# Optimization experiments

Measured on AMD Instinct MI355X. Metric: run time of the kernel, lower is better.

Reference implementation:

```python
import jax, jax.numpy as jnp
import numpy as np

N_EMBD = 1024
N_HEAD = 16
HEAD_DIM = N_EMBD // N_HEAD


def setup_inputs() -> dict:
    key = jax.random.key(0)
    kx, kq, kk, kv, ko = jax.random.split(key, 5)
    B, S = 2, 2048
    return {
        "x": jax.random.normal(kx, (B, S, N_EMBD), dtype=jnp.float32),
        "W_q": jax.random.normal(kq, (N_EMBD, N_EMBD), dtype=jnp.float32),
        "W_k": jax.random.normal(kk, (N_EMBD, N_EMBD), dtype=jnp.float32),
        "W_v": jax.random.normal(kv, (N_EMBD, N_EMBD), dtype=jnp.float32),
        "W_o": jax.random.normal(ko, (N_EMBD, N_EMBD), dtype=jnp.float32),
    }


def reference(x, W_q, W_k, W_v, W_o):
    B, S, E = x.shape
    H, D = N_HEAD, HEAD_DIM
    scale = 1.0 / np.sqrt(D).astype(np.float32)
    # QKV projections, split into heads: (B, H, S, D)
    q = (x @ W_q).reshape(B, S, H, D).transpose(0, 2, 1, 3)
    k = (x @ W_k).reshape(B, S, H, D).transpose(0, 2, 1, 3)
    v = (x @ W_v).reshape(B, S, H, D).transpose(0, 2, 1, 3)
    # scaled scores with causal mask
    scores = jnp.einsum("bhqd,bhkd->bhqk", q, k) * scale
    causal = jnp.tril(jnp.ones((S, S), dtype=bool))
    scores = jnp.where(causal, scores, -jnp.inf)
    attn = jax.nn.softmax(scores, axis=-1)
    out = jnp.einsum("bhqk,bhkd->bhqd", attn, v)
    out = out.transpose(0, 2, 1, 3).reshape(B, S, E)
    return out @ W_o
```

## Files before the change

kernel.cpp:

```cpp
#include <hip/hip_runtime.h>
#include <stdint.h>

#define E 1024
#define S 2048
#define NH 16
#define HD 64

typedef _Float16 f16;
typedef _Float16 f16x4 __attribute__((ext_vector_type(4)));
typedef _Float16 f16x8 __attribute__((ext_vector_type(8)));
typedef __fp16 hv4 __attribute__((ext_vector_type(4)));
typedef float f32x4 __attribute__((ext_vector_type(4)));

__device__ __forceinline__ void async16(const void* g, void* l) {
  __builtin_amdgcn_global_load_lds(
      (const __attribute__((address_space(1))) unsigned int*)g,
      (__attribute__((address_space(3))) unsigned int*)l, 16, 0, 0);
}

__global__ __launch_bounds__(256) void cvt_all(
    const float* __restrict__ x, const float* __restrict__ Wq,
    const float* __restrict__ Wk, const float* __restrict__ Wv,
    const float* __restrict__ Wo, f16* __restrict__ xh, f16* __restrict__ xl,
    f16* __restrict__ Wh, f16* __restrict__ Wl) {
  const int z = blockIdx.z;
  const int tid = threadIdx.x;
  if (z == 4) {
    int base = ((blockIdx.y * 32 + blockIdx.x) * 256 + tid) * 16;
#pragma unroll
    for (int u = 0; u < 4; u++) {
      int i = base + u * 4;
      float4 a = *(const float4*)(x + i);
      f16 h0 = (f16)a.x, h1 = (f16)a.y, h2 = (f16)a.z, h3 = (f16)a.w;
      f16x4 hv = {h0, h1, h2, h3};
      f16x4 lv = {(f16)(a.x - (float)h0), (f16)(a.y - (float)h1),
                  (f16)(a.z - (float)h2), (f16)(a.w - (float)h3)};
      *(f16x4*)(xh + i) = hv;
      *(f16x4*)(xl + i) = lv;
    }
    return;
  }
  __shared__ float tile[32][33];
  const float* W = z == 0 ? Wq : z == 1 ? Wk : z == 2 ? Wv : Wo;
  const int tx = tid & 31, ty = tid >> 5;
  const int x0 = blockIdx.x * 32, y0 = blockIdx.y * 32;
#pragma unroll
  for (int i = 0; i < 4; i++)
    tile[ty + i * 8][tx] = W[(size_t)(y0 + ty + i * 8) * E + x0 + tx];
  __syncthreads();
  f16* outh = Wh + (size_t)z * E * E;
  f16* outl = Wl + (size_t)z * E * E;
#pragma unroll
  for (int i = 0; i < 4; i++) {
    float v = tile[tx][ty + i * 8];
    size_t o = (size_t)(x0 + ty + i * 8) * E + (y0 + tx);
    f16 hi = (f16)v;
    outh[o] = hi;
    if (z < 2) outl[o] = (f16)(v - (float)hi);
  }
}


template <bool SPLIT2>
__device__ __forceinline__ void gemm_mainloop(
    const f16* __restrict__ Ah, const f16* __restrict__ Al,
    const f16* __restrict__ Bh, const f16* __restrict__ Bl, int m0, int n0,
    int K, f16* Ahs, f16* Als, f16* Bhs, f16* Bls, f32x4 acc[4][4]) {
  const int tid = threadIdx.x, lane = tid & 63, wid = tid >> 6;
  const int quad = lane >> 4, c16 = lane & 15;
  const int rA = tid >> 2;
  const int cA = (tid & 3) ^ ((rA >> 1) & 3);
  const size_t gA0 = (size_t)(m0 + rA) * K + cA * 8;
  const size_t gA1 = (size_t)(m0 + 64 + rA) * K + cA * 8;
  const size_t gB0 = (size_t)(n0 + rA) * K + cA * 8;
  const size_t gB1 = (size_t)(n0 + 64 + rA) * K + cA * 8;
  const int l0 = tid * 8, l1 = (256 + tid) * 8;
  int a_off[4], b_off[4];
#pragma unroll
  for (int i = 0; i < 4; i++) {
    int ra = (wid >> 1) * 64 + i * 16 + c16;
    a_off[i] = ra * 32 + ((quad ^ ((ra >> 1) & 3)) << 3);
    int rb = (wid & 1) * 64 + i * 16 + c16;
    b_off[i] = rb * 32 + ((quad ^ ((rb >> 1) & 3)) << 3);
  }
  auto stage = [&](int k0, int b) {
    const int o = b << 12;
    async16(Ah + gA0 + k0, Ahs + o + l0);
    async16(Ah + gA1 + k0, Ahs + o + l1);
    async16(Bh + gB0 + k0, Bhs + o + l0);
    async16(Bh + gB1 + k0, Bhs + o + l1);
    if constexpr (SPLIT2) {
      async16(Al + gA0 + k0, Als + o + l0);
      async16(Al + gA1 + k0, Als + o + l1);
      async16(Bl + gB0 + k0, Bls + o + l0);
      async16(Bl + gB1 + k0, Bls + o + l1);
    }
  };
  stage(0, 0);
  int cur = 0;
  for (int k0 = 0; k0 < K; k0 += 32, cur ^= 1) {
    __syncthreads();
    if (k0 + 32 < K) stage(k0 + 32, cur ^ 1);
    const int o = cur << 12;
    f16x8 ah[4], bh[4];
#pragma unroll
    for (int i = 0; i < 4; i++) {
      ah[i] = *(const f16x8*)(Ahs + o + a_off[i]);
      bh[i] = *(const f16x8*)(Bhs + o + b_off[i]);
    }
    if constexpr (SPLIT2) {
      f16x8 al[4], bl[4];
#pragma unroll
      for (int i = 0; i < 4; i++) {
        al[i] = *(const f16x8*)(Als + o + a_off[i]);
        bl[i] = *(const f16x8*)(Bls + o + b_off[i]);
      }
#pragma unroll
      for (int i = 0; i < 4; i++)
#pragma unroll
        for (int j = 0; j < 4; j++) {
          acc[i][j] = __builtin_amdgcn_mfma_f32_16x16x32_f16(ah[i], bh[j], acc[i][j], 0, 0, 0);
          acc[i][j] = __builtin_amdgcn_mfma_f32_16x16x32_f16(ah[i], bl[j], acc[i][j], 0, 0, 0);
          acc[i][j] = __builtin_amdgcn_mfma_f32_16x16x32_f16(al[i], bh[j], acc[i][j], 0, 0, 0);
        }
    } else {
#pragma unroll
      for (int i = 0; i < 4; i++)
#pragma unroll
        for (int j = 0; j < 4; j++)
          acc[i][j] = __builtin_amdgcn_mfma_f32_16x16x32_f16(ah[i], bh[j], acc[i][j], 0, 0, 0);
    }
  }
}

__global__ __launch_bounds__(256) void qkv_gemm(
    const f16* __restrict__ xh, const f16* __restrict__ xl,
    const f16* __restrict__ Wh, const f16* __restrict__ Wl,
    f16* __restrict__ Qh, f16* __restrict__ Ql, f16* __restrict__ Kh,
    f16* __restrict__ Kl, f16* __restrict__ Vt) {
  __shared__ __align__(16) f16 Ahs[2][4096], Als[2][4096], Bhs[2][4096],
      Bls[2][4096];
  const int z = blockIdx.y >> 3;
  const int m0 = blockIdx.x * 128, n0 = (blockIdx.y & 7) * 128;
  const f16* Bth = Wh + (size_t)z * E * E;
  const f16* Btl = Wl + (size_t)z * E * E;
  f32x4 acc[4][4];
  const f32x4 zero4 = {0.f, 0.f, 0.f, 0.f};
#pragma unroll
  for (int i = 0; i < 4; i++)
#pragma unroll
    for (int j = 0; j < 4; j++) acc[i][j] = zero4;
  if (z < 2)
    gemm_mainloop<true>(xh, xl, Bth, Btl, m0, n0, E, &Ahs[0][0], &Als[0][0],
                        &Bhs[0][0], &Bls[0][0], acc);
  else
    gemm_mainloop<false>(xh, nullptr, Bth, nullptr, m0, n0, E, &Ahs[0][0],
                         nullptr, &Bhs[0][0], nullptr, acc);
  const int tid = threadIdx.x, lane = tid & 63, wid = tid >> 6;
  const int quad = lane >> 4, c16 = lane & 15;
  if (z == 2) {
    __syncthreads();
    f16* vbuf = &Ahs[0][0] + (size_t)wid * 4608;
#pragma unroll
    for (int i = 0; i < 4; i++)
#pragma unroll
      for (int j = 0; j < 4; j++)
#pragma unroll
        for (int r = 0; r < 4; r++) {
          int sl = i * 16 + quad * 4 + r;
          int dl = j * 16 + c16;
          vbuf[dl * 72 + sl] = (f16)acc[i][j][r];
        }
#pragma unroll
    for (int i2 = 0; i2 < 8; i2++) {
      int dl = i2 * 8 + (lane >> 3);
      int ck = lane & 7;
      f16x8 v8 = *(const f16x8*)(vbuf + dl * 72 + ck * 8);
      int dg = n0 + (wid & 1) * 64 + dl;
      int sg = m0 + (wid >> 1) * 64 + ck * 8;
      int b = sg >> 11, s = sg & (S - 1);
      int h = dg >> 6, d = dg & 63;
      *(f16x8*)(Vt + (((size_t)(b * NH + h) * HD + d) << 11) + s) = v8;
    }
  } else {
    const float sc = 0.42466090014400953f;
#pragma unroll
    for (int i = 0; i < 4; i++)
#pragma unroll
      for (int j = 0; j < 4; j++)
#pragma unroll
        for (int r = 0; r < 4; r++) {
          int row = m0 + (wid >> 1) * 64 + i * 16 + quad * 4 + r;
          int col = n0 + (wid & 1) * 64 + j * 16 + c16;
          int b = row >> 11, s = row & (S - 1);
          int h = col >> 6, d = col & 63;
          float v = acc[i][j][r] * sc;
          size_t idx = (((size_t)(b * NH + h) * S + s) << 6) + d;
          f16 hi = (f16)v;
          f16 lo = (f16)(v - (float)hi);
          if (z == 0) { Qh[idx] = hi; Ql[idx] = lo; }
          else        { Kh[idx] = hi; Kl[idx] = lo; }
        }
  }
}

__global__ __launch_bounds__(256, 3) void flash(
    const f16* __restrict__ Qh, const f16* __restrict__ Ql,
    const f16* __restrict__ Kh, const f16* __restrict__ Kl,
    const f16* __restrict__ Vt, f16* __restrict__ Ao) {
  __shared__ __align__(16) f16 Khs[2][4096], Kls[2][4096], Vs[2][4096];
  const int tid = threadIdx.x, lane = tid & 63, wid = tid >> 6;
  const int quad = lane >> 4, c16 = lane & 15;
  const int flat = blockIdx.y * 32 + blockIdx.x;
  const int xcd = flat & 7, slot = flat >> 3;
  const int bh = xcd * 4 + (slot >> 5);
  const int qtile = 31 - (slot & 31);
  const int q0 = qtile * 64;
  const size_t bhoff = (size_t)bh * S * HD;
  const int qbase = wid * 16;
  f16x8 qf_h[2], qf_l[2];
#pragma unroll
  for (int ks = 0; ks < 2; ks++) {
    int q = q0 + qbase + c16;
    size_t off = bhoff + (size_t)q * HD + ks * 32 + quad * 8;
    qf_h[ks] = *(const f16x8*)(Qh + off);
    qf_l[ks] = *(const f16x8*)(Ql + off);
  }
  const int niter = qtile + 1;
  const int s0 = tid, s1 = 256 + tid;
  const int r0 = s0 >> 3, cc0 = ((s0 & 7) ^ (r0 & 7)) * 8;
  const int r1 = s1 >> 3, cc1 = ((s1 & 7) ^ (r1 & 7)) * 8;
  auto stage = [&](int it, int b) {
    const size_t kb = bhoff + (size_t)(it * 64) * HD;
    async16(Kh + kb + r0 * HD + cc0, &Khs[b][s0 * 8]);
    async16(Kh + kb + r1 * HD + cc1, &Khs[b][s1 * 8]);
    async16(Kl + kb + r0 * HD + cc0, &Kls[b][s0 * 8]);
    async16(Kl + kb + r1 * HD + cc1, &Kls[b][s1 * 8]);
    const size_t vb = bhoff + (size_t)(it * 64);
    async16(Vt + vb + (size_t)r0 * S + cc0, &Vs[b][s0 * 8]);
    async16(Vt + vb + (size_t)r1 * S + cc1, &Vs[b][s1 * 8]);
  };
  stage(0, 0);
  float mrow = -3.0e38f, lsum = 0.f;
  f32x4 oacc[4];
  const f32x4 zero4 = {0.f, 0.f, 0.f, 0.f};
#pragma unroll
  for (int dt = 0; dt < 4; dt++) oacc[dt] = zero4;
  const int qrow = q0 + qbase + c16;
  for (int it = 0; it < niter; ++it) {
    const int cur = it & 1;
    __syncthreads();
    if (it + 1 < niter) stage(it + 1, cur ^ 1);
    const int k0 = it * 64;
    f32x4 st[4];
#pragma unroll
    for (int kt = 0; kt < 4; kt++) st[kt] = zero4;
#pragma unroll
    for (int kt = 0; kt < 4; kt++) {
      int rowk = (kt * 16 + c16) * 64;
      int sx = c16 & 7;
      f16x8 kh0 = *(const f16x8*)&Khs[cur][rowk + ((quad ^ sx) << 3)];
      f16x8 kh1 = *(const f16x8*)&Khs[cur][rowk + (((4 + quad) ^ sx) << 3)];
      f16x8 kl0 = *(const f16x8*)&Kls[cur][rowk + ((quad ^ sx) << 3)];
      f16x8 kl1 = *(const f16x8*)&Kls[cur][rowk + (((4 + quad) ^ sx) << 3)];
      st[kt] = __builtin_amdgcn_mfma_f32_16x16x32_f16(kh0, qf_h[0], st[kt], 0, 0, 0);
      st[kt] = __builtin_amdgcn_mfma_f32_16x16x32_f16(kh1, qf_h[1], st[kt], 0, 0, 0);
      st[kt] = __builtin_amdgcn_mfma_f32_16x16x32_f16(kh0, qf_l[0], st[kt], 0, 0, 0);
      st[kt] = __builtin_amdgcn_mfma_f32_16x16x32_f16(kh1, qf_l[1], st[kt], 0, 0, 0);
      st[kt] = __builtin_amdgcn_mfma_f32_16x16x32_f16(kl0, qf_h[0], st[kt], 0, 0, 0);
      st[kt] = __builtin_amdgcn_mfma_f32_16x16x32_f16(kl1, qf_h[1], st[kt], 0, 0, 0);
    }
    if (it == niter - 1) {
#pragma unroll
      for (int kt = 0; kt < 4; kt++) {
        int kb = k0 + kt * 16 + quad * 4;
#pragma unroll
        for (int r = 0; r < 4; r++)
          if (kb + r > qrow) st[kt][r] = -3.0e38f;
      }
    }
    float mx = -3.0e38f;
#pragma unroll
    for (int kt = 0; kt < 4; kt++) {
      float a = fmaxf(fmaxf(st[kt][0], st[kt][1]), fmaxf(st[kt][2], st[kt][3]));
      mx = fmaxf(mx, a);
    }
    mx = fmaxf(mx, __shfl_xor(mx, 16, 64));
    mx = fmaxf(mx, __shfl_xor(mx, 32, 64));
    float mn = fmaxf(mrow, mx);
    float alpha = __builtin_amdgcn_exp2f(mrow - mn);
    mrow = mn;
    float ls = lsum * alpha;
    hv4 pb[4];
#pragma unroll
    for (int kt = 0; kt < 4; kt++) {
      float p0 = __builtin_amdgcn_exp2f(st[kt][0] - mn);
      float p1 = __builtin_amdgcn_exp2f(st[kt][1] - mn);
      float p2 = __builtin_amdgcn_exp2f(st[kt][2] - mn);
      float p3 = __builtin_amdgcn_exp2f(st[kt][3] - mn);
      ls += (p0 + p1) + (p2 + p3);
      hv4 pv = {(__fp16)p0, (__fp16)p1, (__fp16)p2, (__fp16)p3};
      pb[kt] = pv;
    }
    lsum = ls;
#pragma unroll
    for (int dt = 0; dt < 4; dt++) {
      oacc[dt][0] *= alpha;
      oacc[dt][1] *= alpha;
      oacc[dt][2] *= alpha;
      oacc[dt][3] *= alpha;
    }
#pragma unroll
    for (int kt = 0; kt < 4; kt++) {
#pragma unroll
      for (int dt = 0; dt < 4; dt++) {
        int rowd = dt * 16 + c16;
        int cidx = (kt * 2 + (quad >> 1)) ^ (rowd & 7);
        hv4 vf = *(const hv4*)&Vs[cur][rowd * 64 + (cidx << 3) + (quad & 1) * 4];
        oacc[dt] = __builtin_amdgcn_mfma_f32_16x16x16f16(vf, pb[kt], oacc[dt], 0, 0, 0);
      }
    }
  }
  const int bb = bh >> 4, hh = bh & 15;
  float l = lsum;
  l += __shfl_xor(l, 16, 64);
  l += __shfl_xor(l, 32, 64);
  float iv = 1.0f / l;
  const int q = q0 + qbase + c16;
#pragma unroll
  for (int dt = 0; dt < 4; dt++) {
    f16x4 ov = {(f16)(oacc[dt][0] * iv), (f16)(oacc[dt][1] * iv),
                (f16)(oacc[dt][2] * iv), (f16)(oacc[dt][3] * iv)};
    *(f16x4*)(Ao + ((size_t)(bb * S + q)) * E + hh * 64 + dt * 16 + quad * 4) = ov;
  }
}

__global__ __launch_bounds__(256) void out_gemm(const f16* __restrict__ Ao,
                                                const f16* __restrict__ Wo,
                                                float* __restrict__ Cout) {
  __shared__ __align__(16) f16 Ahs[2][2048], Bhs[2][4096];
  const int tid = threadIdx.x, lane = tid & 63, wid = tid >> 6;
  const int quad = lane >> 4, c16 = lane & 15;
  const int m0 = blockIdx.x * 64, n0 = blockIdx.y * 128;
  f32x4 acc[4][2];
  const f32x4 zero4 = {0.f, 0.f, 0.f, 0.f};
#pragma unroll
  for (int i = 0; i < 4; i++)
#pragma unroll
    for (int j = 0; j < 2; j++) acc[i][j] = zero4;
  const int rA = tid >> 2;
  const int cA = (tid & 3) ^ ((rA >> 1) & 3);
  const size_t gA0 = (size_t)(m0 + rA) * E + cA * 8;
  const size_t gB0 = (size_t)(n0 + rA) * E + cA * 8;
  const size_t gB1 = (size_t)(n0 + 64 + rA) * E + cA * 8;
  const int l0 = tid * 8, l1 = (256 + tid) * 8;
  int a_off[4], b_off[2];
#pragma unroll
  for (int i = 0; i < 4; i++) {
    int ra = i * 16 + c16;
    a_off[i] = ra * 32 + ((quad ^ ((ra >> 1) & 3)) << 3);
  }
#pragma unroll
  for (int j = 0; j < 2; j++) {
    int rb = wid * 32 + j * 16 + c16;
    b_off[j] = rb * 32 + ((quad ^ ((rb >> 1) & 3)) << 3);
  }
  auto stage = [&](int k0, int b) {
    async16(Ao + gA0 + k0, &Ahs[b][0] + l0);
    async16(Wo + gB0 + k0, &Bhs[b][0] + l0);
    async16(Wo + gB1 + k0, &Bhs[b][0] + l1);
  };
  stage(0, 0);
  int cur = 0;
  for (int k0 = 0; k0 < E; k0 += 32, cur ^= 1) {
    __syncthreads();
    if (k0 + 32 < E) stage(k0 + 32, cur ^ 1);
    f16x8 ah[4], bh[2];
#pragma unroll
    for (int i = 0; i < 4; i++) ah[i] = *(const f16x8*)(&Ahs[cur][0] + a_off[i]);
#pragma unroll
    for (int j = 0; j < 2; j++) bh[j] = *(const f16x8*)(&Bhs[cur][0] + b_off[j]);
#pragma unroll
    for (int i = 0; i < 4; i++)
#pragma unroll
      for (int j = 0; j < 2; j++)
        acc[i][j] = __builtin_amdgcn_mfma_f32_16x16x32_f16(ah[i], bh[j], acc[i][j], 0, 0, 0);
  }
#pragma unroll
  for (int i = 0; i < 4; i++)
#pragma unroll
    for (int j = 0; j < 2; j++)
#pragma unroll
      for (int r = 0; r < 4; r++) {
        int row = m0 + i * 16 + quad * 4 + r;
        int col = n0 + wid * 32 + j * 16 + c16;
        Cout[(size_t)row * E + col] = acc[i][j][r];
      }
}

extern "C" void kernel_launch(void* const* d_in, const int* in_sizes, int n_in,
                              void* d_out, int out_size, void* d_ws,
                              size_t ws_size, hipStream_t stream) {
  const float* x = (const float*)d_in[0];
  const float* Wq = (const float*)d_in[1];
  const float* Wk = (const float*)d_in[2];
  const float* Wv = (const float*)d_in[3];
  const float* Wo = (const float*)d_in[4];
  char* ws = (char*)d_ws;
  const size_t MB = (size_t)1 << 20;
  f16* xh = (f16*)(ws + 0 * MB);
  f16* xl = (f16*)(ws + 8 * MB);
  f16* Wh = (f16*)(ws + 16 * MB);
  f16* Wl = (f16*)(ws + 24 * MB);
  f16* Qh = (f16*)(ws + 28 * MB);
  f16* Ql = (f16*)(ws + 36 * MB);
  f16* Kh = (f16*)(ws + 44 * MB);
  f16* Kl = (f16*)(ws + 52 * MB);
  f16* Vt = (f16*)(ws + 60 * MB);
  f16* Ao = (f16*)(ws + 68 * MB);
  cvt_all<<<dim3(32, 32, 5), 256, 0, stream>>>(x, Wq, Wk, Wv, Wo, xh, xl, Wh, Wl);
  qkv_gemm<<<dim3(32, 24), 256, 0, stream>>>(xh, xl, Wh, Wl, Qh, Ql, Kh, Kl, Vt);
  flash<<<dim3(32, 32), 256, 0, stream>>>(Qh, Ql, Kh, Kl, Vt, Ao);
  out_gemm<<<dim3(64, 8), 256, 0, stream>>>(Ao, Wh + (size_t)3 * E * E, (float*)d_out);
}
```

Baseline: 236.4 us.

## Pair complementary causal query tiles per flash block to balance work and share K/V

```diff
diff --git a/kernel.cpp b/kernel.cpp
--- a/kernel.cpp
+++ b/kernel.cpp
@@ -204,29 +204,31 @@
   }
 }
 
-__global__ __launch_bounds__(256, 3) void flash(
+__global__ __launch_bounds__(256, 2) void flash(
     const f16* __restrict__ Qh, const f16* __restrict__ Ql,
     const f16* __restrict__ Kh, const f16* __restrict__ Kl,
     const f16* __restrict__ Vt, f16* __restrict__ Ao) {
   __shared__ __align__(16) f16 Khs[2][4096], Kls[2][4096], Vs[2][4096];
   const int tid = threadIdx.x, lane = tid & 63, wid = tid >> 6;
   const int quad = lane >> 4, c16 = lane & 15;
-  const int flat = blockIdx.y * 32 + blockIdx.x;
+  const int flat = blockIdx.y * 16 + blockIdx.x;
   const int xcd = flat & 7, slot = flat >> 3;
-  const int bh = xcd * 4 + (slot >> 5);
-  const int qtile = 31 - (slot & 31);
-  const int q0 = qtile * 64;
+  const int bh = xcd * 4 + (slot >> 4);
+  const int t = slot & 15;
+  const int q0A = t * 64, q0B = (31 - t) * 64;
+  const int nA = t + 1, nB = 32 - t;
   const size_t bhoff = (size_t)bh * S * HD;
   const int qbase = wid * 16;
-  f16x8 qf_h[2], qf_l[2];
+  f16x8 qfA_h[2], qfA_l[2], qfB_h[2], qfB_l[2];
 #pragma unroll
   for (int ks = 0; ks < 2; ks++) {
-    int q = q0 + qbase + c16;
-    size_t off = bhoff + (size_t)q * HD + ks * 32 + quad * 8;
-    qf_h[ks] = *(const f16x8*)(Qh + off);
-    qf_l[ks] = *(const f16x8*)(Ql + off);
-  }
-  const int niter = qtile + 1;
+    size_t offA = bhoff + (size_t)(q0A + qbase + c16) * HD + ks * 32 + quad * 8;
+    size_t offB = bhoff + (size_t)(q0B + qbase + c16) * HD + ks * 32 + quad * 8;
+    qfA_h[ks] = *(const f16x8*)(Qh + offA);
+    qfA_l[ks] = *(const f16x8*)(Ql + offA);
+    qfB_h[ks] = *(const f16x8*)(Qh + offB);
+    qfB_l[ks] = *(const f16x8*)(Ql + offB);
+  }
   const int s0 = tid, s1 = 256 + tid;
   const int r0 = s0 >> 3, cc0 = ((s0 & 7) ^ (r0 & 7)) * 8;
   const int r1 = s1 >> 3, cc1 = ((s1 & 7) ^ (r1 & 7)) * 8;
@@ -241,20 +243,21 @@
     async16(Vt + vb + (size_t)r1 * S + cc1, &Vs[b][s1 * 8]);
   };
   stage(0, 0);
-  float mrow = -3.0e38f, lsum = 0.f;
-  f32x4 oacc[4];
+  float mrowA = -3.0e38f, lsumA = 0.f, mrowB = -3.0e38f, lsumB = 0.f;
+  f32x4 oaccA[4], oaccB[4];
   const f32x4 zero4 = {0.f, 0.f, 0.f, 0.f};
 #pragma unroll
-  for (int dt = 0; dt < 4; dt++) oacc[dt] = zero4;
-  const int qrow = q0 + qbase + c16;
-  for (int it = 0; it < niter; ++it) {
+  for (int dt = 0; dt < 4; dt++) { oaccA[dt] = zero4; oaccB[dt] = zero4; }
+  const int qrowA = q0A + qbase + c16, qrowB = q0B + qbase + c16;
+  for (int it = 0; it < nB; ++it) {
     const int cur = it & 1;
     __syncthreads();
-    if (it + 1 < niter) stage(it + 1, cur ^ 1);
+    if (it + 1 < nB) stage(it + 1, cur ^ 1);
+    const bool doA = (it < nA);
     const int k0 = it * 64;
-    f32x4 st[4];
-#pragma unroll
-    for (int kt = 0; kt < 4; kt++) st[kt] = zero4;
+    f32x4 stA[4], stB[4];
+#pragma unroll
+    for (int kt = 0; kt < 4; kt++) { stA[kt] = zero4; stB[kt] = zero4; }
 #pragma unroll
     for (int kt = 0; kt < 4; kt++) {
       int rowk = (kt * 16 + c16) * 64;
@@ -263,52 +266,97 @@
       f16x8 kh1 = *(const f16x8*)&Khs[cur][rowk + (((4 + quad) ^ sx) << 3)];
       f16x8 kl0 = *(const f16x8*)&Kls[cur][rowk + ((quad ^ sx) << 3)];
       f16x8 kl1 = *(const f16x8*)&Kls[cur][rowk + (((4 + quad) ^ sx) << 3)];
-      st[kt] = __builtin_amdgcn_mfma_f32_16x16x32_f16(kh0, qf_h[0], st[kt], 0, 0, 0);
-      st[kt] = __builtin_amdgcn_mfma_f32_16x16x32_f16(kh1, qf_h[1], st[kt], 0, 0, 0);
-      st[kt] = __builtin_amdgcn_mfma_f32_16x16x32_f16(kh0, qf_l[0], st[kt], 0, 0, 0);
-      st[kt] = __builtin_amdgcn_mfma_f32_16x16x32_f16(kh1, qf_l[1], st[kt], 0, 0, 0);
-      st[kt] = __builtin_amdgcn_mfma_f32_16x16x32_f16(kl0, qf_h[0], st[kt], 0, 0, 0);
-      st[kt] = __builtin_amdgcn_mfma_f32_16x16x32_f16(kl1, qf_h[1], st[kt], 0, 0, 0);
-    }
-    if (it == niter - 1) {
+      stB[kt] = __builtin_amdgcn_mfma_f32_16x16x32_f16(kh0, qfB_h[0], stB[kt], 0, 0, 0);
+      stB[kt] = __builtin_amdgcn_mfma_f32_16x16x32_f16(kh1, qfB_h[1], stB[kt], 0, 0, 0);
+      stB[kt] = __builtin_amdgcn_mfma_f32_16x16x32_f16(kh0, qfB_l[0], stB[kt], 0, 0, 0);
+      stB[kt] = __builtin_amdgcn_mfma_f32_16x16x32_f16(kh1, qfB_l[1], stB[kt], 0, 0, 0);
+      stB[kt] = __builtin_amdgcn_mfma_f32_16x16x32_f16(kl0, qfB_h[0], stB[kt], 0, 0, 0);
+      stB[kt] = __builtin_amdgcn_mfma_f32_16x16x32_f16(kl1, qfB_h[1], stB[kt], 0, 0, 0);
+      if (doA) {
+        stA[kt] = __builtin_amdgcn_mfma_f32_16x16x32_f16(kh0, qfA_h[0], stA[kt], 0, 0, 0);
+        stA[kt] = __builtin_amdgcn_mfma_f32_16x16x32_f16(kh1, qfA_h[1], stA[kt], 0, 0, 0);
+        stA[kt] = __builtin_amdgcn_mfma_f32_16x16x32_f16(kh0, qfA_l[0], stA[kt], 0, 0, 0);
+        stA[kt] = __builtin_amdgcn_mfma_f32_16x16x32_f16(kh1, qfA_l[1], stA[kt], 0, 0, 0);
+        stA[kt] = __builtin_amdgcn_mfma_f32_16x16x32_f16(kl0, qfA_h[0], stA[kt], 0, 0, 0);
+        stA[kt] = __builtin_amdgcn_mfma_f32_16x16x32_f16(kl1, qfA_h[1], stA[kt], 0, 0, 0);
+      }
+    }
+    hv4 pbA[4], pbB[4];
+    {
+      if (it == nB - 1) {
+#pragma unroll
+        for (int kt = 0; kt < 4; kt++) {
+          int kb = k0 + kt * 16 + quad * 4;
+#pragma unroll
+          for (int r = 0; r < 4; r++)
+            if (kb + r > qrowB) stB[kt][r] = -3.0e38f;
+        }
+      }
+      float mx = -3.0e38f;
+#pragma unroll
+      for (int kt = 0; kt < 4; kt++)
+        mx = fmaxf(mx, fmaxf(fmaxf(stB[kt][0], stB[kt][1]),
+                             fmaxf(stB[kt][2], stB[kt][3])));
+      mx = fmaxf(mx, __shfl_xor(mx, 16, 64));
+      mx = fmaxf(mx, __shfl_xor(mx, 32, 64));
+      float mn = fmaxf(mrowB, mx);
+      float alpha = __builtin_amdgcn_exp2f(mrowB - mn);
+      mrowB = mn;
+      float ls = lsumB * alpha;
 #pragma unroll
       for (int kt = 0; kt < 4; kt++) {
-        int kb = k0 + kt * 16 + quad * 4;
-#pragma unroll
-        for (int r = 0; r < 4; r++)
-          if (kb + r > qrow) st[kt][r] = -3.0e38f;
-      }
-    }
-    float mx = -3.0e38f;
-#pragma unroll
-    for (int kt = 0; kt < 4; kt++) {
-      float a = fmaxf(fmaxf(st[kt][0], st[kt][1]), fmaxf(st[kt][2], st[kt][3]));
-      mx = fmaxf(mx, a);
-    }
-    mx = fmaxf(mx, __shfl_xor(mx, 16, 64));
-    mx = fmaxf(mx, __shfl_xor(mx, 32, 64));
-    float mn = fmaxf(mrow, mx);
-    float alpha = __builtin_amdgcn_exp2f(mrow - mn);
-    mrow = mn;
-    float ls = lsum * alpha;
-    hv4 pb[4];
-#pragma unroll
-    for (int kt = 0; kt < 4; kt++) {
-      float p0 = __builtin_amdgcn_exp2f(st[kt][0] - mn);
-      float p1 = __builtin_amdgcn_exp2f(st[kt][1] - mn);
-      float p2 = __builtin_amdgcn_exp2f(st[kt][2] - mn);
-      float p3 = __builtin_amdgcn_exp2f(st[kt][3] - mn);
-      ls += (p0 + p1) + (p2 + p3);
-      hv4 pv = {(__fp16)p0, (__fp16)p1, (__fp16)p2, (__fp16)p3};
-      pb[kt] = pv;
-    }
-    lsum = ls;
-#pragma unroll
-    for (int dt = 0; dt < 4; dt++) {
-      oacc[dt][0] *= alpha;
-      oacc[dt][1] *= alpha;
-      oacc[dt][2] *= alpha;
-      oacc[dt][3] *= alpha;
+        float p0 = __builtin_amdgcn_exp2f(stB[kt][0] - mn);
+        float p1 = __builtin_amdgcn_exp2f(stB[kt][1] - mn);
+        float p2 = __builtin_amdgcn_exp2f(stB[kt][2] - mn);
+        float p3 = __builtin_amdgcn_exp2f(stB[kt][3] - mn);
+        ls += (p0 + p1) + (p2 + p3);
+        hv4 pv = {(__fp16)p0, (__fp16)p1, (__fp16)p2, (__fp16)p3};
+        pbB[kt] = pv;
+      }
+      lsumB = ls;
+#pragma unroll
+      for (int dt = 0; dt < 4; dt++) {
+        oaccB[dt][0] *= alpha; oaccB[dt][1] *= alpha;
+        oaccB[dt][2] *= alpha; oaccB[dt][3] *= alpha;
+      }
+    }
+    if (doA) {
+      if (it == nA - 1) {
+#pragma unroll
+        for (int kt = 0; kt < 4; kt++) {
+          int kb = k0 + kt * 16 + quad * 4;
+#pragma unroll
+          for (int r = 0; r < 4; r++)
+            if (kb + r > qrowA) stA[kt][r] = -3.0e38f;
+        }
+      }
+      float mx = -3.0e38f;
+#pragma unroll
+      for (int kt = 0; kt < 4; kt++)
+        mx = fmaxf(mx, fmaxf(fmaxf(stA[kt][0], stA[kt][1]),
+                             fmaxf(stA[kt][2], stA[kt][3])));
+      mx = fmaxf(mx, __shfl_xor(mx, 16, 64));
+      mx = fmaxf(mx, __shfl_xor(mx, 32, 64));
+      float mn = fmaxf(mrowA, mx);
+      float alpha = __builtin_amdgcn_exp2f(mrowA - mn);
+      mrowA = mn;
+      float ls = lsumA * alpha;
+#pragma unroll
+      for (int kt = 0; kt < 4; kt++) {
+        float p0 = __builtin_amdgcn_exp2f(stA[kt][0] - mn);
+        float p1 = __builtin_amdgcn_exp2f(stA[kt][1] - mn);
+        float p2 = __builtin_amdgcn_exp2f(stA[kt][2] - mn);
+        float p3 = __builtin_amdgcn_exp2f(stA[kt][3] - mn);
+        ls += (p0 + p1) + (p2 + p3);
+        hv4 pv = {(__fp16)p0, (__fp16)p1, (__fp16)p2, (__fp16)p3};
+        pbA[kt] = pv;
+      }
+      lsumA = ls;
+#pragma unroll
+      for (int dt = 0; dt < 4; dt++) {
+        oaccA[dt][0] *= alpha; oaccA[dt][1] *= alpha;
+        oaccA[dt][2] *= alpha; oaccA[dt][3] *= alpha;
+      }
     }
 #pragma unroll
     for (int kt = 0; kt < 4; kt++) {
@@ -317,21 +365,26 @@
         int rowd = dt * 16 + c16;
         int cidx = (kt * 2 + (quad >> 1)) ^ (rowd & 7);
         hv4 vf = *(const hv4*)&Vs[cur][rowd * 64 + (cidx << 3) + (quad & 1) * 4];
-        oacc[dt] = __builtin_amdgcn_mfma_f32_16x16x16f16(vf, pb[kt], oacc[dt], 0, 0, 0);
+        oaccB[dt] = __builtin_amdgcn_mfma_f32_16x16x16f16(vf, pbB[kt], oaccB[dt], 0, 0, 0);
+        if (doA)
+          oaccA[dt] = __builtin_amdgcn_mfma_f32_16x16x16f16(vf, pbA[kt], oaccA[dt], 0, 0, 0);
       }
     }
   }
   const int bb = bh >> 4, hh = bh & 15;
-  float l = lsum;
-  l += __shfl_xor(l, 16, 64);
-  l += __shfl_xor(l, 32, 64);
-  float iv = 1.0f / l;
-  const int q = q0 + qbase + c16;
+  float lA = lsumA, lB = lsumB;
+  lA += __shfl_xor(lA, 16, 64); lA += __shfl_xor(lA, 32, 64);
+  lB += __shfl_xor(lB, 16, 64); lB += __shfl_xor(lB, 32, 64);
+  float ivA = 1.0f / lA, ivB = 1.0f / lB;
+  const int qA = q0A + qbase + c16, qB = q0B + qbase + c16;
 #pragma unroll
   for (int dt = 0; dt < 4; dt++) {
-    f16x4 ov = {(f16)(oacc[dt][0] * iv), (f16)(oacc[dt][1] * iv),
-                (f16)(oacc[dt][2] * iv), (f16)(oacc[dt][3] * iv)};
-    *(f16x4*)(Ao + ((size_t)(bb * S + q)) * E + hh * 64 + dt * 16 + quad * 4) = ov;
+    f16x4 ovA = {(f16)(oaccA[dt][0] * ivA), (f16)(oaccA[dt][1] * ivA),
+                 (f16)(oaccA[dt][2] * ivA), (f16)(oaccA[dt][3] * ivA)};
+    f16x4 ovB = {(f16)(oaccB[dt][0] * ivB), (f16)(oaccB[dt][1] * ivB),
+                 (f16)(oaccB[dt][2] * ivB), (f16)(oaccB[dt][3] * ivB)};
+    *(f16x4*)(Ao + ((size_t)(bb * S + qA)) * E + hh * 64 + dt * 16 + quad * 4) = ovA;
+    *(f16x4*)(Ao + ((size_t)(bb * S + qB)) * E + hh * 64 + dt * 16 + quad * 4) = ovB;
   }
 }
 
@@ -420,6 +473,6 @@
   f16* Ao = (f16*)(ws + 68 * MB);
   cvt_all<<<dim3(32, 32, 5), 256, 0, stream>>>(x, Wq, Wk, Wv, Wo, xh, xl, Wh, Wl);
   qkv_gemm<<<dim3(32, 24), 256, 0, stream>>>(xh, xl, Wh, Wl, Qh, Ql, Kh, Kl, Vt);
-  flash<<<dim3(32, 32), 256, 0, stream>>>(Qh, Ql, Kh, Kl, Vt, Ao);
+  flash<<<dim3(16, 32), 256, 0, stream>>>(Qh, Ql, Kh, Kl, Vt, Ao);
   out_gemm<<<dim3(64, 8), 256, 0, stream>>>(Ao, Wh + (size_t)3 * E * E, (float*)d_out);
 }
```

After: 251.5 us. 6.4% more time.

## Load K-low fragments to registers directly and compute row sums via MFMA

Applied to the files above, without the earlier changes.

```diff
diff --git a/kernel.cpp b/kernel.cpp
--- a/kernel.cpp
+++ b/kernel.cpp
@@ -204,11 +204,11 @@
   }
 }
 
-__global__ __launch_bounds__(256, 3) void flash(
+__global__ __launch_bounds__(256, 4) void flash(
     const f16* __restrict__ Qh, const f16* __restrict__ Ql,
     const f16* __restrict__ Kh, const f16* __restrict__ Kl,
     const f16* __restrict__ Vt, f16* __restrict__ Ao) {
-  __shared__ __align__(16) f16 Khs[2][4096], Kls[2][4096], Vs[2][4096];
+  __shared__ __align__(16) f16 Khs[2][4096], Vs[2][4096];
   const int tid = threadIdx.x, lane = tid & 63, wid = tid >> 6;
   const int quad = lane >> 4, c16 = lane & 15;
   const int flat = blockIdx.y * 32 + blockIdx.x;
@@ -234,18 +234,29 @@
     const size_t kb = bhoff + (size_t)(it * 64) * HD;
     async16(Kh + kb + r0 * HD + cc0, &Khs[b][s0 * 8]);
     async16(Kh + kb + r1 * HD + cc1, &Khs[b][s1 * 8]);
-    async16(Kl + kb + r0 * HD + cc0, &Kls[b][s0 * 8]);
-    async16(Kl + kb + r1 * HD + cc1, &Kls[b][s1 * 8]);
     const size_t vb = bhoff + (size_t)(it * 64);
     async16(Vt + vb + (size_t)r0 * S + cc0, &Vs[b][s0 * 8]);
     async16(Vt + vb + (size_t)r1 * S + cc1, &Vs[b][s1 * 8]);
   };
+  const f16* klp = Kl + bhoff + c16 * 64 + quad * 8;
+  f16x8 klr[8];
+  auto load_kl = [&](int it) {
+#pragma unroll
+    for (int kt = 0; kt < 4; kt++) {
+      klr[kt * 2 + 0] = *(const f16x8*)(klp + it * 4096 + kt * 1024);
+      klr[kt * 2 + 1] = *(const f16x8*)(klp + it * 4096 + kt * 1024 + 32);
+    }
+  };
   stage(0, 0);
-  float mrow = -3.0e38f, lsum = 0.f;
+  load_kl(0);
+  float mrow = -3.0e38f;
   f32x4 oacc[4];
+  f32x4 lacc;
   const f32x4 zero4 = {0.f, 0.f, 0.f, 0.f};
+  const hv4 ones4 = {(__fp16)1.f, (__fp16)1.f, (__fp16)1.f, (__fp16)1.f};
 #pragma unroll
   for (int dt = 0; dt < 4; dt++) oacc[dt] = zero4;
+  lacc = zero4;
   const int qrow = q0 + qbase + c16;
   for (int it = 0; it < niter; ++it) {
     const int cur = it & 1;
@@ -261,14 +272,15 @@
       int sx = c16 & 7;
       f16x8 kh0 = *(const f16x8*)&Khs[cur][rowk + ((quad ^ sx) << 3)];
       f16x8 kh1 = *(const f16x8*)&Khs[cur][rowk + (((4 + quad) ^ sx) << 3)];
-      f16x8 kl0 = *(const f16x8*)&Kls[cur][rowk + ((quad ^ sx) << 3)];
-      f16x8 kl1 = *(const f16x8*)&Kls[cur][rowk + (((4 + quad) ^ sx) << 3)];
       st[kt] = __builtin_amdgcn_mfma_f32_16x16x32_f16(kh0, qf_h[0], st[kt], 0, 0, 0);
       st[kt] = __builtin_amdgcn_mfma_f32_16x16x32_f16(kh1, qf_h[1], st[kt], 0, 0, 0);
       st[kt] = __builtin_amdgcn_mfma_f32_16x16x32_f16(kh0, qf_l[0], st[kt], 0, 0, 0);
       st[kt] = __builtin_amdgcn_mfma_f32_16x16x32_f16(kh1, qf_l[1], st[kt], 0, 0, 0);
-      st[kt] = __builtin_amdgcn_mfma_f32_16x16x32_f16(kl0, qf_h[0], st[kt], 0, 0, 0);
-      st[kt] = __builtin_amdgcn_mfma_f32_16x16x32_f16(kl1, qf_h[1], st[kt], 0, 0, 0);
+    }
+#pragma unroll
+    for (int kt = 0; kt < 4; kt++) {
+      st[kt] = __builtin_amdgcn_mfma_f32_16x16x32_f16(klr[kt * 2 + 0], qf_h[0], st[kt], 0, 0, 0);
+      st[kt] = __builtin_amdgcn_mfma_f32_16x16x32_f16(klr[kt * 2 + 1], qf_h[1], st[kt], 0, 0, 0);
     }
     if (it == niter - 1) {
 #pragma unroll
@@ -290,7 +302,6 @@
     float mn = fmaxf(mrow, mx);
     float alpha = __builtin_amdgcn_exp2f(mrow - mn);
     mrow = mn;
-    float ls = lsum * alpha;
     hv4 pb[4];
 #pragma unroll
     for (int kt = 0; kt < 4; kt++) {
@@ -298,11 +309,9 @@
       float p1 = __builtin_amdgcn_exp2f(st[kt][1] - mn);
       float p2 = __builtin_amdgcn_exp2f(st[kt][2] - mn);
       float p3 = __builtin_amdgcn_exp2f(st[kt][3] - mn);
-      ls += (p0 + p1) + (p2 + p3);
       hv4 pv = {(__fp16)p0, (__fp16)p1, (__fp16)p2, (__fp16)p3};
       pb[kt] = pv;
     }
-    lsum = ls;
 #pragma unroll
     for (int dt = 0; dt < 4; dt++) {
       oacc[dt][0] *= alpha;
@@ -310,8 +319,10 @@
       oacc[dt][2] *= alpha;
       oacc[dt][3] *= alpha;
     }
-#pragma unroll
-    for (int kt = 0; kt < 4; kt++) {
+    lacc[0] *= alpha; lacc[1] *= alpha; lacc[2] *= alpha; lacc[3] *= alpha;
+#pragma unroll
+    for (int kt = 0; kt < 4; kt++) {
+      lacc = __builtin_amdgcn_mfma_f32_16x16x16f16(ones4, pb[kt], lacc, 0, 0, 0);
 #pragma unroll
       for (int dt = 0; dt < 4; dt++) {
         int rowd = dt * 16 + c16;
@@ -320,12 +331,10 @@
         oacc[dt] = __builtin_amdgcn_mfma_f32_16x16x16f16(vf, pb[kt], oacc[dt], 0, 0, 0);
       }
     }
+    if (it + 1 < niter) load_kl(it + 1);
   }
   const int bb = bh >> 4, hh = bh & 15;
-  float l = lsum;
-  l += __shfl_xor(l, 16, 64);
-  l += __shfl_xor(l, 32, 64);
-  float iv = 1.0f / l;
+  float iv = 1.0f / lacc[0];
   const int q = q0 + qbase + c16;
 #pragma unroll
   for (int dt = 0; dt < 4; dt++) {
```

Measured after the change: 311.4 us. +31.7%, slower.
